# Optimization experiments

Hardware: AMD Instinct MI355X
Metric: run time of the kernel (lower is better)

## Reference

```python
import jax, jax.numpy as jnp
import numpy as np

B, S, D, H, DH, FF = 2, 2048, 1024, 16, 64, 4096
EPS = 1e-6


def setup_inputs() -> dict:
    key = jax.random.key(0)
    ks = jax.random.split(key, 12)
    s = lambda fan: 1.0 / np.sqrt(fan)
    return {
        "x": jax.random.normal(ks[0], (B, S, D), dtype=jnp.float32),
        "mask": jax.random.randint(ks[1], (B, S), 0, 2).astype(bool),
        "Wq": jax.random.normal(ks[2], (D, H * DH), dtype=jnp.float32) * s(D),
        "Wk": jax.random.normal(ks[3], (D, H * DH), dtype=jnp.float32) * s(D),
        "Wv": jax.random.normal(ks[4], (D, H * DH), dtype=jnp.float32) * s(D),
        "Wo": jax.random.normal(ks[5], (H * DH, D), dtype=jnp.float32) * s(H * DH),
        "bo": jnp.zeros((D,), dtype=jnp.float32),
        "W1": jax.random.normal(ks[6], (D, FF), dtype=jnp.float32) * s(D),
        "b1": jnp.zeros((FF,), dtype=jnp.float32),
        "W2": jax.random.normal(ks[7], (FF, D), dtype=jnp.float32) * s(FF),
        "b2": jnp.zeros((D,), dtype=jnp.float32),
        "g1": jnp.ones((D,), dtype=jnp.float32),   # layer_norm1 target_std
        "m1": jnp.zeros((D,), dtype=jnp.float32),  # layer_norm1 target_mean
        "g2": jnp.ones((D,), dtype=jnp.float32),
        "m2": jnp.zeros((D,), dtype=jnp.float32),
    }


def layer_norm(x, g, m):
    mu = jnp.mean(x, axis=-1, keepdims=True)
    xc = x - mu
    std = jnp.sqrt(jnp.mean(xc * xc, axis=-1, keepdims=True) + EPS)
    return g * xc / std + m


def reference(x, mask, Wq, Wk, Wv, Wo, bo, W1, b1, W2, b2, g1, m1, g2, m2):
    # --- multi-head self-attention (no proj bias) ---
    q = (x @ Wq).reshape(B, S, H, DH)
    k = (x @ Wk).reshape(B, S, H, DH)
    v = (x @ Wv).reshape(B, S, H, DH)
    scores = jnp.einsum("bqhd,bkhd->bhqk", q, k) / np.sqrt(DH)  # [B,H,S,S]
    scores = jnp.where(mask[:, None, None, :], -jnp.inf, scores)
    att = jax.nn.softmax(scores, axis=-1)
    ctx = jnp.einsum("bhqk,bkhd->bqhd", att, v).reshape(B, S, H * DH)
    attn_out = ctx @ Wo + bo
    # --- post-LN residual block (pre_ln=False, dropouts=0 in eval) ---
    x1 = layer_norm(attn_out + x, g1, m1)
    ff = jax.nn.relu(x1 @ W1 + b1) @ W2 + b2
    return layer_norm(ff + x1, g2, m2)
```

## Files before the change

### kernel.cpp

```cpp
#include <hip/hip_runtime.h>
#include <hip/hip_bf16.h>


typedef __bf16 bf16;
typedef __bf16 bf16x8 __attribute__((ext_vector_type(8)));
typedef __bf16 bf16x4 __attribute__((ext_vector_type(4)));
typedef float  f32x4  __attribute__((ext_vector_type(4)));
typedef float  f32x16 __attribute__((ext_vector_type(16)));
typedef unsigned u32x2 __attribute__((ext_vector_type(2)));
typedef unsigned u32x4 __attribute__((ext_vector_type(4)));

#define DEVI __device__ __forceinline__

constexpr int S_LEN  = 2048;
constexpr int NTOK   = 4096;
constexpr int DMODEL = 1024;
constexpr int NFF    = 4096;
constexpr float SCALE2 = 0.125f * 1.44269504088896f;
constexpr float MASKV2 = -30000.0f;

DEVI void gld16(const void* g, void* l) {
  __builtin_amdgcn_global_load_lds((const __attribute__((address_space(1))) void*)g,
                                   (__attribute__((address_space(3))) void*)l, 16, 0, 0);
}

DEVI f32x4 mfma16(bf16x8 a, bf16x8 b, f32x4 c) {
  return __builtin_amdgcn_mfma_f32_16x16x32_bf16(a, b, c, 0, 0, 0);
}
DEVI f32x16 mfma32(bf16x8 a, bf16x8 b, f32x16 c) {
  return __builtin_amdgcn_mfma_f32_32x32x16_bf16(a, b, c, 0, 0, 0);
}
DEVI unsigned cvtpk(float lo, float hi) {
  unsigned d;
  asm("v_cvt_pk_bf16_f32 %0, %1, %2" : "=v"(d) : "v"(lo), "v"(hi));
  return d;
}
DEVI void plswap(unsigned &a, unsigned &b) {
#if __has_builtin(__builtin_amdgcn_permlane32_swap)
  u32x2 r = __builtin_amdgcn_permlane32_swap(a, b, false, false);
  a = r[0]; b = r[1];
#else
  asm volatile("v_permlane32_swap_b32 %0, %1" : "+v"(a), "+v"(b));
#endif
}
DEVI float fexp2(float x) {
#if __has_builtin(__builtin_amdgcn_exp2f)
  return __builtin_amdgcn_exp2f(x);
#else
  return exp2f(x);
#endif
}

template <int MODE>
__global__ __launch_bounds__(256) void gemm_bt(
    const bf16* __restrict__ A, const bf16* __restrict__ Bt,
    void* __restrict__ out, const float* __restrict__ bias,
    int M, int N, int ld, int Kc, int nx, int ny)
{
  __shared__ bf16 As[128 * 32];
  __shared__ bf16 Bs[128 * 32];
  const int tid  = threadIdx.x;
  const int lane = tid & 63, w = tid >> 6;
  const int wr = w >> 1, wc = w & 1;

  const int id  = blockIdx.x;
  const int xcd = id & 7;
  int t2 = id >> 3;
  const int bx = t2 % nx;  t2 /= nx;
  const int ppx = ny >> 3;
  const int kz = t2 / ppx;
  const int by = xcd * ppx + (t2 % ppx);
  const int brow = by * 128, bcol = bx * 128;

  const bf16* Ag = A  + (size_t)(brow + w * 32 + (lane >> 2)) * ld + kz * Kc + (lane & 3) * 8;
  const bf16* Bg = Bt + (size_t)(bcol + w * 32 + (lane >> 2)) * ld + kz * Kc + (lane & 3) * 8;
  bf16* AsW = As + w * 1024;
  bf16* BsW = Bs + w * 1024;

  f32x4 acc[4][4] = {};

  for (int k0 = 0; k0 < Kc; k0 += 32) {
    gld16(Ag + k0,                    AsW);
    gld16(Ag + k0 + (size_t)16 * ld,  AsW + 512);
    gld16(Bg + k0,                    BsW);
    gld16(Bg + k0 + (size_t)16 * ld,  BsW + 512);
    __syncthreads();

    bf16x8 af[4], bfr[4];
#pragma unroll
    for (int m = 0; m < 4; ++m)
      af[m] = *(const bf16x8*)&As[(wr * 64 + m * 16 + (lane & 15)) * 32 + (lane >> 4) * 8];
#pragma unroll
    for (int n = 0; n < 4; ++n)
      bfr[n] = *(const bf16x8*)&Bs[(wc * 64 + n * 16 + (lane & 15)) * 32 + (lane >> 4) * 8];
    __builtin_amdgcn_s_setprio(1);
#pragma unroll
    for (int m = 0; m < 4; ++m)
#pragma unroll
      for (int n = 0; n < 4; ++n)
        acc[m][n] = mfma16(af[m], bfr[n], acc[m][n]);
    __builtin_amdgcn_s_setprio(0);
    __syncthreads();
  }

  const size_t plane = (size_t)NTOK * DMODEL;
#pragma unroll
  for (int m = 0; m < 4; ++m)
#pragma unroll
    for (int n = 0; n < 4; ++n)
#pragma unroll
      for (int r = 0; r < 4; ++r) {
        const int row = brow + wr * 64 + m * 16 + (lane >> 4) * 4 + r;
        const int col = bcol + wc * 64 + n * 16 + (lane & 15);
        const float v = acc[m][n][r];
        if (MODE == 0) {
          const int b = row >> 11, s = row & 2047;
          const int which = col >> 10, c = col & 1023, h = c >> 6, d = c & 63;
          bf16* qkv = (bf16*)out;
          if (which == 0)
            qkv[(((size_t)(b * 16 + h)) * 2048 + s) * 64 + d] = (bf16)v;
          else if (which == 1)
            (qkv + plane)[(((size_t)(b * 16 + h)) * 2048 + s) * 64 + d] = (bf16)v;
          else
            (qkv + 2 * plane)[(((size_t)(b * 16 + h)) * 64 + d) * 2048 + s] = (bf16)v;
        } else if (MODE == 3) {
          const float t = v + bias[col];
          ((bf16*)out)[(size_t)row * N + col] = (bf16)fmaxf(t, 0.0f);
        } else {
          ((float*)out)[(size_t)kz * M * N + (size_t)row * N + col] = v;
        }
      }
}

__global__ __launch_bounds__(512) void attn_k(
    const bf16* __restrict__ q, const bf16* __restrict__ k,
    const bf16* __restrict__ vt, const unsigned* __restrict__ mbits,
    bf16* __restrict__ ctx)
{
  __shared__ __align__(16) char smem[36864];
  bf16* Kl = (bf16*)smem;
  bf16* Vl = (bf16*)(smem + 16384);
  const int tid = threadIdx.x, lane = tid & 63, w = tid >> 6;
  const int hi = lane >> 5, li = lane & 31;
  const int bh = blockIdx.y, b = bh >> 4, h = bh & 15;
  const int qbase = blockIdx.x * 256 + w * 32;

  bf16x8 qf[4];
  {
    const bf16* qp = q + ((size_t)bh * S_LEN + qbase + li) * 64 + hi * 8;
#pragma unroll
    for (int c = 0; c < 4; ++c) qf[c] = *(const bf16x8*)(qp + c * 16);
  }

  f32x16 o[2] = {};
  float mrun = -3.0e38f, lrun = 0.f;

  const int srow = w * 8 + (lane >> 3);
  const int sslot = (lane & 7) ^ ((srow ^ (srow >> 3)) & 7);
  const bf16* kg = k  + ((size_t)bh * S_LEN + srow) * 64 + sslot * 8;
  const bf16* vg = vt + ((size_t)bh * 64 + srow) * S_LEN + sslot * 8;

  gld16(kg, Kl + w * 512);
  gld16(vg, Vl + w * 512);
  __syncthreads();

  int buf = 0;
  for (int kt = 0; kt < 32; ++kt) {
    const int nb = buf ^ 1;
    if (kt + 1 < 32) {
      gld16(kg + (size_t)(kt + 1) * 4096, Kl + nb * 4096 + w * 512);
      gld16(vg + (kt + 1) * 64,           Vl + nb * 4096 + w * 512);
    }
    const unsigned mw0 = mbits[b * 64 + kt * 2]     >> (hi * 4);
    const unsigned mw1 = mbits[b * 64 + kt * 2 + 1] >> (hi * 4);
    const bf16* Kb = Kl + buf * 4096;
    const bf16* Vb = Vl + buf * 4096;

    float sc[2][16];
#pragma unroll
    for (int kblk = 0; kblk < 2; ++kblk) {
      const int key = kblk * 32 + li;
      const unsigned swb = ((key ^ (key >> 3)) & 7) << 4;
      const char* kr = (const char*)Kb + key * 128;
      f32x16 st = {};
      __builtin_amdgcn_s_setprio(1);
#pragma unroll
      for (int c = 0; c < 4; ++c) {
        const bf16x8 kf = *(const bf16x8*)(kr + ((unsigned)(c * 32 + hi * 16) ^ swb));
        st = mfma32(kf, qf[c], st);
      }
      __builtin_amdgcn_s_setprio(0);
      const unsigned msh = kblk ? mw1 : mw0;
#pragma unroll
      for (int r = 0; r < 16; ++r) {
        const int cb = (r & 3) + 8 * (r >> 2);
        const float v = st[r] * SCALE2;
        sc[kblk][r] = (msh & (1u << cb)) ? MASKV2 : v;
      }
    }

    float tm = fmaxf(sc[0][0], sc[1][0]);
#pragma unroll
    for (int r = 1; r < 16; ++r) tm = fmaxf(tm, fmaxf(sc[0][r], sc[1][r]));
    tm = fmaxf(tm, __shfl_xor(tm, 32, 64));
    const float mnew = fmaxf(mrun, tm);
    const float alpha = fexp2(mrun - mnew);
    mrun = mnew;
    float rsum = 0.f;
#pragma unroll
    for (int kblk = 0; kblk < 2; ++kblk)
#pragma unroll
      for (int r = 0; r < 16; ++r) {
        const float p = fexp2(sc[kblk][r] - mnew);
        sc[kblk][r] = p;
        rsum += p;
      }
    rsum += __shfl_xor(rsum, 32, 64);
    lrun = lrun * alpha + rsum;
    o[0] *= alpha;
    o[1] *= alpha;

    bf16x8 pa[4];
#pragma unroll
    for (int kblk = 0; kblk < 2; ++kblk)
#pragma unroll
      for (int hf = 0; hf < 2; ++hf) {
        unsigned A = cvtpk(sc[kblk][hf * 8 + 0], sc[kblk][hf * 8 + 1]);
        unsigned B = cvtpk(sc[kblk][hf * 8 + 2], sc[kblk][hf * 8 + 3]);
        unsigned C = cvtpk(sc[kblk][hf * 8 + 4], sc[kblk][hf * 8 + 5]);
        unsigned D = cvtpk(sc[kblk][hf * 8 + 6], sc[kblk][hf * 8 + 7]);
        plswap(A, C);
        plswap(B, D);
        const u32x4 t = {A, B, C, D};
        pa[kblk * 2 + hf] = __builtin_bit_cast(bf16x8, t);
      }

#pragma unroll
    for (int dblk = 0; dblk < 2; ++dblk) {
      const int d = dblk * 32 + li;
      const unsigned swb = ((d ^ (d >> 3)) & 7) << 4;
      const char* vr = (const char*)Vb + d * 128;
      __builtin_amdgcn_s_setprio(1);
#pragma unroll
      for (int ch = 0; ch < 4; ++ch) {
        const bf16x8 vf = *(const bf16x8*)(vr + ((unsigned)(ch * 32 + hi * 16) ^ swb));
        o[dblk] = mfma32(vf, pa[ch], o[dblk]);
      }
      __builtin_amdgcn_s_setprio(0);
    }
    __syncthreads();
    buf = nb;
  }

  const float rl = 1.0f / lrun;
  char* Ep = smem + w * 4608;
#pragma unroll
  for (int dblk = 0; dblk < 2; ++dblk)
#pragma unroll
    for (int g = 0; g < 4; ++g) {
      const unsigned lo = cvtpk(o[dblk][4 * g + 0] * rl, o[dblk][4 * g + 1] * rl);
      const unsigned hw = cvtpk(o[dblk][4 * g + 2] * rl, o[dblk][4 * g + 3] * rl);
      const int d0 = 8 * g + 4 * hi + 32 * dblk;
      *(unsigned long long*)(Ep + li * 144 + d0 * 2) =
          ((unsigned long long)hw << 32) | (unsigned long long)lo;
    }
#pragma unroll
  for (int i = 0; i < 4; ++i) {
    const int r = (lane >> 3) + 8 * i;
    const bf16x8 vv = *(const bf16x8*)(Ep + r * 144 + (lane & 7) * 16);
    *(bf16x8*)(ctx + ((size_t)b * S_LEN + qbase + r) * DMODEL + h * 64 + (lane & 7) * 8) = vv;
  }
}

template <int NPART, int RB>
__global__ __launch_bounds__(256) void ln_k(
    const float* __restrict__ parts, const float* __restrict__ bias,
    const void* __restrict__ resid, const float* __restrict__ gam,
    const float* __restrict__ bet, float* __restrict__ of, bf16* __restrict__ ob)
{
  const int row = blockIdx.x, t = threadIdx.x;
  float4 v = ((const float4*)(parts + (size_t)row * DMODEL))[t];
#pragma unroll
  for (int p = 1; p < NPART; ++p) {
    const float4 u = ((const float4*)(parts + ((size_t)p * NTOK + row) * DMODEL))[t];
    v.x += u.x; v.y += u.y; v.z += u.z; v.w += u.w;
  }
  {
    const float4 b4 = ((const float4*)bias)[t];
    float4 r4;
    if (RB) {
      const bf16x4 rb = *(const bf16x4*)((const bf16*)resid + (size_t)row * DMODEL + t * 4);
      r4.x = (float)rb[0]; r4.y = (float)rb[1]; r4.z = (float)rb[2]; r4.w = (float)rb[3];
    } else {
      r4 = ((const float4*)((const float*)resid + (size_t)row * DMODEL))[t];
    }
    v.x += b4.x + r4.x; v.y += b4.y + r4.y; v.z += b4.z + r4.z; v.w += b4.w + r4.w;
  }
  float s  = v.x + v.y + v.z + v.w;
  float s2 = v.x * v.x + v.y * v.y + v.z * v.z + v.w * v.w;
#pragma unroll
  for (int off = 1; off < 64; off <<= 1) {
    s  += __shfl_xor(s, off, 64);
    s2 += __shfl_xor(s2, off, 64);
  }
  __shared__ float ps[4], ps2[4];
  if ((t & 63) == 0) { ps[t >> 6] = s; ps2[t >> 6] = s2; }
  __syncthreads();
  s  = ps[0] + ps[1] + ps[2] + ps[3];
  s2 = ps2[0] + ps2[1] + ps2[2] + ps2[3];
  const float mu   = s * (1.f / 1024.f);
  const float var  = fmaxf(s2 * (1.f / 1024.f) - mu * mu, 0.f);
  const float rstd = rsqrtf(var + 1e-6f);
  const float4 g4 = ((const float4*)gam)[t];
  const float4 b4 = ((const float4*)bet)[t];
  float4 ov;
  ov.x = g4.x * (v.x - mu) * rstd + b4.x;
  ov.y = g4.y * (v.y - mu) * rstd + b4.y;
  ov.z = g4.z * (v.z - mu) * rstd + b4.z;
  ov.w = g4.w * (v.w - mu) * rstd + b4.w;
  if (of) ((float4*)(of + (size_t)row * DMODEL))[t] = ov;
  if (ob) {
    const bf16x4 o4 = {(bf16)ov.x, (bf16)ov.y, (bf16)ov.z, (bf16)ov.w};
    *(bf16x4*)(ob + (size_t)row * DMODEL + t * 4) = o4;
  }
}

__global__ __launch_bounds__(256) void f2b_k(const float* __restrict__ in,
                                             bf16* __restrict__ out, int n4)
{
  const int i = blockIdx.x * 256 + threadIdx.x;
  if (i >= n4) return;
  const float4 v = ((const float4*)in)[i];
  const bf16x4 o = {(bf16)v.x, (bf16)v.y, (bf16)v.z, (bf16)v.w};
  *(bf16x4*)(out + (size_t)i * 4) = o;
}

__global__ __launch_bounds__(256) void tconv_k(const float* __restrict__ in,
                                               bf16* __restrict__ out, int K, int N)
{
  __shared__ float tile[32][33];
  const int tx = threadIdx.x & 31, ty = threadIdx.x >> 5;
  const int r0 = blockIdx.y * 32, c0 = blockIdx.x * 32;
#pragma unroll
  for (int i = 0; i < 32; i += 8)
    tile[ty + i][tx] = in[(size_t)(r0 + ty + i) * N + c0 + tx];
  __syncthreads();
#pragma unroll
  for (int i = 0; i < 32; i += 8)
    out[(size_t)(c0 + ty + i) * K + r0 + tx] = (bf16)tile[tx][ty + i];
}

__global__ __launch_bounds__(256) void mask_conv_k(const void* __restrict__ m,
                                                   unsigned* __restrict__ mbits)
{
  __shared__ int s_gt1, s_f1;
  const int t = threadIdx.x;
  if (t == 0) { s_gt1 = 0; s_f1 = 0; }
  __syncthreads();
  const unsigned int* wds = (const unsigned int*)m;
  int gt1 = 0, f1 = 0;
  for (int i = t; i < 1024; i += 256) {
    const unsigned int x = wds[i];
    gt1 |= (x > 1u);
    f1  |= (x == 0x3F800000u);
  }
  if (gt1) atomicOr(&s_gt1, 1);
  if (f1)  atomicOr(&s_f1, 1);
  __syncthreads();
  const int md = s_f1 ? 2 : (s_gt1 ? 1 : 0);
  if (t < NTOK / 32) {
    unsigned wd = 0;
    for (int j = 0; j < 32; ++j) {
      const int e = t * 32 + j;
      unsigned mv;
      if (md == 1)      mv = (((const unsigned char*)m)[e] != 0);
      else if (md == 2) mv = (((const float*)m)[e] != 0.f);
      else              mv = (((const int*)m)[e] != 0);
      wd |= mv << j;
    }
    mbits[t] = wd;
  }
}

extern "C" void kernel_launch(void* const* d_in, const int* in_sizes, int n_in,
                              void* d_out, int out_size, void* d_ws, size_t ws_size,
                              hipStream_t stream)
{
  const float* x    = (const float*)d_in[0];
  const void*  mask = d_in[1];
  const float* Wq   = (const float*)d_in[2];
  const float* Wk   = (const float*)d_in[3];
  const float* Wv   = (const float*)d_in[4];
  const float* Wo   = (const float*)d_in[5];
  const float* bo   = (const float*)d_in[6];
  const float* W1   = (const float*)d_in[7];
  const float* b1   = (const float*)d_in[8];
  const float* W2   = (const float*)d_in[9];
  const float* b2   = (const float*)d_in[10];
  const float* g1   = (const float*)d_in[11];
  const float* m1   = (const float*)d_in[12];
  const float* g2   = (const float*)d_in[13];
  const float* m2   = (const float*)d_in[14];

  const size_t plane = (size_t)NTOK * DMODEL;
  const int split = (ws_size >= (size_t)140 * 1024 * 1024) ? 4 : 2;

  char* ws = (char*)d_ws;
  size_t off = 0;
  auto alloc = [&](size_t bytes) {
    char* p = ws + off;
    off += (bytes + 255) & ~(size_t)255;
    return p;
  };
  char* region0 = alloc((size_t)16 * 1024 * 1024 + 1024);
  bf16* xb     = (bf16*)region0;
  bf16* WqkvT  = (bf16*)(region0 + plane * 2);
  bf16* WoT    = (bf16*)(region0 + plane * 2 + (size_t)3 * DMODEL * DMODEL * 2);

  bf16* W1T  = (bf16*)alloc((size_t)NFF * DMODEL * 2);
  bf16* W2T  = (bf16*)alloc((size_t)DMODEL * NFF * 2);
  bf16* qkv  = (bf16*)alloc(4 * plane * 2);
  bf16* qb = qkv, *kb = qkv + plane, *vtb = qkv + 2 * plane, *ctxb = qkv + 3 * plane;
  bf16* hb   = qkv;
  float* parts = (float*)alloc((size_t)split * plane * 4);
  bf16*  x1b   = (bf16*)alloc(plane * 2);
  unsigned* maskbits = (unsigned*)alloc(512);

  f2b_k<<<dim3(4096), dim3(256), 0, stream>>>(x, xb, NTOK * DMODEL / 4);
  tconv_k<<<dim3(32, 32),  dim3(256), 0, stream>>>(Wq, WqkvT, DMODEL, DMODEL);
  tconv_k<<<dim3(32, 32),  dim3(256), 0, stream>>>(Wk, WqkvT + (size_t)DMODEL * DMODEL, DMODEL, DMODEL);
  tconv_k<<<dim3(32, 32),  dim3(256), 0, stream>>>(Wv, WqkvT + (size_t)2 * DMODEL * DMODEL, DMODEL, DMODEL);
  tconv_k<<<dim3(32, 32),  dim3(256), 0, stream>>>(Wo, WoT, DMODEL, DMODEL);
  tconv_k<<<dim3(128, 32), dim3(256), 0, stream>>>(W1, W1T, DMODEL, NFF);
  tconv_k<<<dim3(32, 128), dim3(256), 0, stream>>>(W2, W2T, NFF, DMODEL);
  mask_conv_k<<<dim3(1), dim3(256), 0, stream>>>(mask, maskbits);

  gemm_bt<0><<<dim3(768), dim3(256), 0, stream>>>(
      xb, WqkvT, qkv, nullptr, NTOK, 3 * DMODEL, DMODEL, DMODEL, 24, 32);

  attn_k<<<dim3(S_LEN / 256, 32), dim3(512), 0, stream>>>(qb, kb, vtb, maskbits, ctxb);

  gemm_bt<4><<<dim3(512), dim3(256), 0, stream>>>(
      ctxb, WoT, parts, nullptr, NTOK, DMODEL, DMODEL, DMODEL / 2, 8, 32);
  ln_k<2, 0><<<dim3(NTOK), dim3(256), 0, stream>>>(parts, bo, x, g1, m1, nullptr, x1b);

  gemm_bt<3><<<dim3(1024), dim3(256), 0, stream>>>(
      x1b, W1T, hb, b1, NTOK, NFF, DMODEL, DMODEL, 32, 32);
  gemm_bt<4><<<dim3(256 * split), dim3(256), 0, stream>>>(
      hb, W2T, parts, nullptr, NTOK, DMODEL, NFF, NFF / split, 8, 32);
  if (split == 4)
    ln_k<4, 1><<<dim3(NTOK), dim3(256), 0, stream>>>(parts, b2, x1b, g2, m2, (float*)d_out, nullptr);
  else
    ln_k<2, 1><<<dim3(NTOK), dim3(256), 0, stream>>>(parts, b2, x1b, g2, m2, (float*)d_out, nullptr);
}
```

Before: 282.7 us.

## Fuse prep kernels, lazy softmax rescale, MFMA row sums, XCD-aware attention grid

Merges the x conversion, six weight transpose-converts and the mask conversion into one launch to cut launch overhead. In attention, the softmax scale is folded into Q at the QKV GEMM epilogue. The running max is rescaled only when it grows by more than a threshold, and the row sum is computed with an MFMA against a ones vector instead of VALU adds. The attention grid is remapped so blocks sharing a head land on the same XCD. The FFN2 split-K is fixed at 2. Lazy rescaling risks larger bf16 P values, up to 2^11, which can cost precision.

Result: faster. 271.9 us (-3.8%).

```diff
diff --git a/kernel.cpp b/kernel.cpp
--- a/kernel.cpp
+++ b/kernel.cpp
@@ -50,6 +50,7 @@
   return exp2f(x);
 #endif
 }
+#define M3(a, b, c) fmaxf(fmaxf(a, b), c)
 
 template <int MODE>
 __global__ __launch_bounds__(256) void gemm_bt(
@@ -118,7 +119,7 @@
           const int which = col >> 10, c = col & 1023, h = c >> 6, d = c & 63;
           bf16* qkv = (bf16*)out;
           if (which == 0)
-            qkv[(((size_t)(b * 16 + h)) * 2048 + s) * 64 + d] = (bf16)v;
+            qkv[(((size_t)(b * 16 + h)) * 2048 + s) * 64 + d] = (bf16)(v * SCALE2);
           else if (which == 1)
             (qkv + plane)[(((size_t)(b * 16 + h)) * 2048 + s) * 64 + d] = (bf16)v;
           else
@@ -142,8 +143,11 @@
   bf16* Vl = (bf16*)(smem + 16384);
   const int tid = threadIdx.x, lane = tid & 63, w = tid >> 6;
   const int hi = lane >> 5, li = lane & 31;
-  const int bh = blockIdx.y, b = bh >> 4, h = bh & 15;
-  const int qbase = blockIdx.x * 256 + w * 32;
+  const int id = blockIdx.x;
+  const int j = id >> 3;
+  const int bh = (id & 7) * 4 + (j & 3);
+  const int b = bh >> 4, h = bh & 15;
+  const int qbase = (j >> 2) * 256 + w * 32;
 
   bf16x8 qf[4];
   {
@@ -151,9 +155,12 @@
 #pragma unroll
     for (int c = 0; c < 4; ++c) qf[c] = *(const bf16x8*)(qp + c * 16);
   }
+  const u32x4 onesu = {0x3F803F80u, 0x3F803F80u, 0x3F803F80u, 0x3F803F80u};
+  const bf16x8 onesv = __builtin_bit_cast(bf16x8, onesu);
 
   f32x16 o[2] = {};
-  float mrun = -3.0e38f, lrun = 0.f;
+  f32x16 acc1 = {};
+  float mrun = -3.0e38f;
 
   const int srow = w * 8 + (lane >> 3);
   const int sslot = (lane & 7) ^ ((srow ^ (srow >> 3)) & 7);
@@ -194,31 +201,32 @@
 #pragma unroll
       for (int r = 0; r < 16; ++r) {
         const int cb = (r & 3) + 8 * (r >> 2);
-        const float v = st[r] * SCALE2;
-        sc[kblk][r] = (msh & (1u << cb)) ? MASKV2 : v;
-      }
-    }
-
-    float tm = fmaxf(sc[0][0], sc[1][0]);
-#pragma unroll
-    for (int r = 1; r < 16; ++r) tm = fmaxf(tm, fmaxf(sc[0][r], sc[1][r]));
+        sc[kblk][r] = (msh & (1u << cb)) ? MASKV2 : st[r];
+      }
+    }
+
+    const float* sf = &sc[0][0];
+    float m0[11];
+#pragma unroll
+    for (int i3 = 0; i3 < 10; ++i3) m0[i3] = M3(sf[i3 * 3], sf[i3 * 3 + 1], sf[i3 * 3 + 2]);
+    m0[10] = fmaxf(sf[30], sf[31]);
+    float tm = fmaxf(fmaxf(M3(m0[0], m0[1], m0[2]), M3(m0[3], m0[4], m0[5])),
+                     fmaxf(M3(m0[6], m0[7], m0[8]), fmaxf(m0[9], m0[10])));
     tm = fmaxf(tm, __shfl_xor(tm, 32, 64));
-    const float mnew = fmaxf(mrun, tm);
-    const float alpha = fexp2(mrun - mnew);
-    mrun = mnew;
-    float rsum = 0.f;
+
+    if (!__all(tm <= mrun + 11.0f)) {
+      const float mnew = fmaxf(mrun, tm);
+      const float alpha = fexp2(mrun - mnew);
+      mrun = mnew;
+      o[0] *= alpha;
+      o[1] *= alpha;
+      acc1[0] = acc1[0] * alpha;
+    }
 #pragma unroll
     for (int kblk = 0; kblk < 2; ++kblk)
 #pragma unroll
-      for (int r = 0; r < 16; ++r) {
-        const float p = fexp2(sc[kblk][r] - mnew);
-        sc[kblk][r] = p;
-        rsum += p;
-      }
-    rsum += __shfl_xor(rsum, 32, 64);
-    lrun = lrun * alpha + rsum;
-    o[0] *= alpha;
-    o[1] *= alpha;
+      for (int r = 0; r < 16; ++r)
+        sc[kblk][r] = fexp2(sc[kblk][r] - mrun);
 
     bf16x8 pa[4];
 #pragma unroll
@@ -248,11 +256,13 @@
       }
       __builtin_amdgcn_s_setprio(0);
     }
+#pragma unroll
+    for (int ch = 0; ch < 4; ++ch) acc1 = mfma32(onesv, pa[ch], acc1);
     __syncthreads();
     buf = nb;
   }
 
-  const float rl = 1.0f / lrun;
+  const float rl = 1.0f / acc1[0];
   char* Ep = smem + w * 4608;
 #pragma unroll
   for (int dblk = 0; dblk < 2; ++dblk)
@@ -325,61 +335,79 @@
   }
 }
 
-__global__ __launch_bounds__(256) void f2b_k(const float* __restrict__ in,
-                                             bf16* __restrict__ out, int n4)
-{
-  const int i = blockIdx.x * 256 + threadIdx.x;
-  if (i >= n4) return;
-  const float4 v = ((const float4*)in)[i];
-  const bf16x4 o = {(bf16)v.x, (bf16)v.y, (bf16)v.z, (bf16)v.w};
-  *(bf16x4*)(out + (size_t)i * 4) = o;
-}
-
-__global__ __launch_bounds__(256) void tconv_k(const float* __restrict__ in,
-                                               bf16* __restrict__ out, int K, int N)
+__global__ __launch_bounds__(256) void prep_k(
+    const float* __restrict__ x, const float* __restrict__ Wq,
+    const float* __restrict__ Wk, const float* __restrict__ Wv,
+    const float* __restrict__ Wo, const float* __restrict__ W1,
+    const float* __restrict__ W2, const void* __restrict__ mask,
+    bf16* __restrict__ xb, bf16* __restrict__ WqkvT, bf16* __restrict__ WoT,
+    bf16* __restrict__ W1T, bf16* __restrict__ W2T, unsigned* __restrict__ mbits)
 {
   __shared__ float tile[32][33];
-  const int tx = threadIdx.x & 31, ty = threadIdx.x >> 5;
-  const int r0 = blockIdx.y * 32, c0 = blockIdx.x * 32;
+  __shared__ int s_gt1, s_f1;
+  const int tid = threadIdx.x;
+  const int id = blockIdx.x;
+
+  if (id < 4096) {
+    const int i = id * 256 + tid;
+    const float4 v = ((const float4*)x)[i];
+    const bf16x4 o = {(bf16)v.x, (bf16)v.y, (bf16)v.z, (bf16)v.w};
+    *(bf16x4*)(xb + (size_t)i * 4) = o;
+    return;
+  }
+  if (id == 16384) {
+    if (tid == 0) { s_gt1 = 0; s_f1 = 0; }
+    __syncthreads();
+    const unsigned* wds = (const unsigned*)mask;
+    int gt1 = 0, f1 = 0;
+    for (int i = tid; i < 1024; i += 256) {
+      const unsigned xw = wds[i];
+      gt1 |= (xw > 1u);
+      f1  |= (xw == 0x3F800000u);
+    }
+    if (gt1) atomicOr(&s_gt1, 1);
+    if (f1)  atomicOr(&s_f1, 1);
+    __syncthreads();
+    const int md = s_f1 ? 2 : (s_gt1 ? 1 : 0);
+    if (tid < NTOK / 32) {
+      unsigned wd = 0;
+      for (int jj = 0; jj < 32; ++jj) {
+        const int e = tid * 32 + jj;
+        unsigned mv;
+        if (md == 1)      mv = (((const unsigned char*)mask)[e] != 0);
+        else if (md == 2) mv = (((const float*)mask)[e] != 0.f);
+        else              mv = (((const int*)mask)[e] != 0);
+        wd |= mv << jj;
+      }
+      mbits[tid] = wd;
+    }
+    return;
+  }
+  const float* src; bf16* dst; int K, N, bx, by;
+  if (id < 7168) {
+    int s2 = id - 4096; const int wq = s2 >> 10; s2 &= 1023;
+    src = wq == 0 ? Wq : (wq == 1 ? Wk : Wv);
+    dst = WqkvT + (size_t)wq * DMODEL * DMODEL;
+    K = 1024; N = 1024; bx = s2 & 31; by = s2 >> 5;
+  } else if (id < 8192) {
+    const int s2 = id - 7168;
+    src = Wo; dst = WoT; K = 1024; N = 1024; bx = s2 & 31; by = s2 >> 5;
+  } else if (id < 12288) {
+    const int s2 = id - 8192;
+    src = W1; dst = W1T; K = 1024; N = 4096; bx = s2 & 127; by = s2 >> 7;
+  } else {
+    const int s2 = id - 12288;
+    src = W2; dst = W2T; K = 4096; N = 1024; bx = s2 & 31; by = s2 >> 5;
+  }
+  const int tx = tid & 31, ty = tid >> 5;
+  const int r0 = by * 32, c0 = bx * 32;
 #pragma unroll
   for (int i = 0; i < 32; i += 8)
-    tile[ty + i][tx] = in[(size_t)(r0 + ty + i) * N + c0 + tx];
+    tile[ty + i][tx] = src[(size_t)(r0 + ty + i) * N + c0 + tx];
   __syncthreads();
 #pragma unroll
   for (int i = 0; i < 32; i += 8)
-    out[(size_t)(c0 + ty + i) * K + r0 + tx] = (bf16)tile[tx][ty + i];
-}
-
-__global__ __launch_bounds__(256) void mask_conv_k(const void* __restrict__ m,
-                                                   unsigned* __restrict__ mbits)
-{
-  __shared__ int s_gt1, s_f1;
-  const int t = threadIdx.x;
-  if (t == 0) { s_gt1 = 0; s_f1 = 0; }
-  __syncthreads();
-  const unsigned int* wds = (const unsigned int*)m;
-  int gt1 = 0, f1 = 0;
-  for (int i = t; i < 1024; i += 256) {
-    const unsigned int x = wds[i];
-    gt1 |= (x > 1u);
-    f1  |= (x == 0x3F800000u);
-  }
-  if (gt1) atomicOr(&s_gt1, 1);
-  if (f1)  atomicOr(&s_f1, 1);
-  __syncthreads();
-  const int md = s_f1 ? 2 : (s_gt1 ? 1 : 0);
-  if (t < NTOK / 32) {
-    unsigned wd = 0;
-    for (int j = 0; j < 32; ++j) {
-      const int e = t * 32 + j;
-      unsigned mv;
-      if (md == 1)      mv = (((const unsigned char*)m)[e] != 0);
-      else if (md == 2) mv = (((const float*)m)[e] != 0.f);
-      else              mv = (((const int*)m)[e] != 0);
-      wd |= mv << j;
-    }
-    mbits[t] = wd;
-  }
+    dst[(size_t)(c0 + ty + i) * K + r0 + tx] = (bf16)tile[tx][ty + i];
 }
 
 extern "C" void kernel_launch(void* const* d_in, const int* in_sizes, int n_in,
@@ -403,7 +431,6 @@
   const float* m2   = (const float*)d_in[14];
 
   const size_t plane = (size_t)NTOK * DMODEL;
-  const int split = (ws_size >= (size_t)140 * 1024 * 1024) ? 4 : 2;
 
   char* ws = (char*)d_ws;
   size_t off = 0;
@@ -412,33 +439,25 @@
     off += (bytes + 255) & ~(size_t)255;
     return p;
   };
-  char* region0 = alloc((size_t)16 * 1024 * 1024 + 1024);
-  bf16* xb     = (bf16*)region0;
-  bf16* WqkvT  = (bf16*)(region0 + plane * 2);
-  bf16* WoT    = (bf16*)(region0 + plane * 2 + (size_t)3 * DMODEL * DMODEL * 2);
-
-  bf16* W1T  = (bf16*)alloc((size_t)NFF * DMODEL * 2);
-  bf16* W2T  = (bf16*)alloc((size_t)DMODEL * NFF * 2);
-  bf16* qkv  = (bf16*)alloc(4 * plane * 2);
+  bf16* xb     = (bf16*)alloc(plane * 2);
+  bf16* WqkvT  = (bf16*)alloc((size_t)3 * DMODEL * DMODEL * 2);
+  bf16* WoT    = (bf16*)alloc((size_t)DMODEL * DMODEL * 2);
+  bf16* W1T    = (bf16*)alloc((size_t)NFF * DMODEL * 2);
+  bf16* W2T    = (bf16*)alloc((size_t)DMODEL * NFF * 2);
+  bf16* qkv    = (bf16*)alloc(4 * plane * 2);
   bf16* qb = qkv, *kb = qkv + plane, *vtb = qkv + 2 * plane, *ctxb = qkv + 3 * plane;
-  bf16* hb   = qkv;
-  float* parts = (float*)alloc((size_t)split * plane * 4);
+  bf16* hb     = qkv;
+  float* parts = (float*)alloc(2 * plane * 4);
   bf16*  x1b   = (bf16*)alloc(plane * 2);
   unsigned* maskbits = (unsigned*)alloc(512);
 
-  f2b_k<<<dim3(4096), dim3(256), 0, stream>>>(x, xb, NTOK * DMODEL / 4);
-  tconv_k<<<dim3(32, 32),  dim3(256), 0, stream>>>(Wq, WqkvT, DMODEL, DMODEL);
-  tconv_k<<<dim3(32, 32),  dim3(256), 0, stream>>>(Wk, WqkvT + (size_t)DMODEL * DMODEL, DMODEL, DMODEL);
-  tconv_k<<<dim3(32, 32),  dim3(256), 0, stream>>>(Wv, WqkvT + (size_t)2 * DMODEL * DMODEL, DMODEL, DMODEL);
-  tconv_k<<<dim3(32, 32),  dim3(256), 0, stream>>>(Wo, WoT, DMODEL, DMODEL);
-  tconv_k<<<dim3(128, 32), dim3(256), 0, stream>>>(W1, W1T, DMODEL, NFF);
-  tconv_k<<<dim3(32, 128), dim3(256), 0, stream>>>(W2, W2T, NFF, DMODEL);
-  mask_conv_k<<<dim3(1), dim3(256), 0, stream>>>(mask, maskbits);
+  prep_k<<<dim3(16385), dim3(256), 0, stream>>>(
+      x, Wq, Wk, Wv, Wo, W1, W2, mask, xb, WqkvT, WoT, W1T, W2T, maskbits);
 
   gemm_bt<0><<<dim3(768), dim3(256), 0, stream>>>(
       xb, WqkvT, qkv, nullptr, NTOK, 3 * DMODEL, DMODEL, DMODEL, 24, 32);
 
-  attn_k<<<dim3(S_LEN / 256, 32), dim3(512), 0, stream>>>(qb, kb, vtb, maskbits, ctxb);
+  attn_k<<<dim3(256), dim3(512), 0, stream>>>(qb, kb, vtb, maskbits, ctxb);
 
   gemm_bt<4><<<dim3(512), dim3(256), 0, stream>>>(
       ctxb, WoT, parts, nullptr, NTOK, DMODEL, DMODEL, DMODEL / 2, 8, 32);
@@ -446,10 +465,7 @@
 
   gemm_bt<3><<<dim3(1024), dim3(256), 0, stream>>>(
       x1b, W1T, hb, b1, NTOK, NFF, DMODEL, DMODEL, 32, 32);
-  gemm_bt<4><<<dim3(256 * split), dim3(256), 0, stream>>>(
-      hb, W2T, parts, nullptr, NTOK, DMODEL, NFF, NFF / split, 8, 32);
-  if (split == 4)
-    ln_k<4, 1><<<dim3(NTOK), dim3(256), 0, stream>>>(parts, b2, x1b, g2, m2, (float*)d_out, nullptr);
-  else
-    ln_k<2, 1><<<dim3(NTOK), dim3(256), 0, stream>>>(parts, b2, x1b, g2, m2, (float*)d_out, nullptr);
-}
+  gemm_bt<4><<<dim3(512), dim3(256), 0, stream>>>(
+      hb, W2T, parts, nullptr, NTOK, DMODEL, NFF, NFF / 2, 8, 32);
+  ln_k<2, 1><<<dim3(NTOK), dim3(256), 0, stream>>>(parts, b2, x1b, g2, m2, (float*)d_out, nullptr);
+}
```
